# Performance work log

Hardware: AMD Instinct MI355X
Metric: run time of the kernel (lower is better)

## Reference

```python
import jax, jax.numpy as jnp
import numpy as np

EPS = 1e-8

def setup_inputs() -> dict:
    key = jax.random.key(0)
    k1, k2, k3, k4 = jax.random.split(key, 4)
    N, D = 65536, 384
    x_candidates = jax.random.normal(k1, (N, D), dtype=jnp.float32)
    y = jax.random.normal(k2, (D,), dtype=jnp.float32)
    z = jax.random.normal(k3, (D,), dtype=jnp.float32)
    a = jax.random.normal(k4, (D, D, D), dtype=jnp.float32)
    return {"x_candidates": x_candidates, "y": y, "z": z, "a": a}

def reference(x_candidates, y, z, a):
    # feature_fn is identity: fy = y, fz = z, fx = each candidate row.
    fy, fz = y, z
    # context[i] = sum_{j,k} a[i,j,k] * fy[j] * fz[k]  (the triple loop, fused)
    # computed as two matvecs to avoid materializing a*fy*fz outer products:
    # tmp[i,j] = sum_k a[i,j,k] * fz[k]; context[i] = sum_j tmp[i,j] * fy[j]
    context = jnp.einsum("ij,j->i", jnp.einsum("ijk,k->ij", a, fz), fy)  # [D]
    # denominator = sum_{j,k} a[0,j,k]*fy[j]*fz[k] == context[0]
    denominator = context[0]
    # score(x) = sum_i fx[i] * context[i] / (denominator + eps)
    scores = (x_candidates @ context) / (denominator + EPS)  # [N]
    return scores
```

## Files before the change

kernel.cpp:

```cpp
#include <hip/hip_runtime.h>

#define EPS 1e-8f

constexpr int D = 384;
constexpr int Q_PER_I = (D * D) / 4;
constexpr int P = 4;
constexpr int Q_PER_PART = Q_PER_I / P;
constexpr int THREADS_A = 256;
constexpr int ITERS_A = Q_PER_PART / THREADS_A;
constexpr int J_PER_PART = Q_PER_PART / (D / 4);

__global__ __launch_bounds__(THREADS_A) void ctx_partial_kernel(
    const float* __restrict__ a,
    const float* __restrict__ y,
    const float* __restrict__ z,
    float* __restrict__ partials) {
  const int b = blockIdx.x;
  const int i = b / P;
  const int part = b - i * P;
  const float4* a4 = reinterpret_cast<const float4*>(a) +
                     (size_t)i * Q_PER_I + (size_t)part * Q_PER_PART;
  const float4* z4 = reinterpret_cast<const float4*>(z);
  const int jbase = part * J_PER_PART;
  const int tid = threadIdx.x;

  float acc = 0.0f;
#pragma unroll 4
  for (int it = 0; it < ITERS_A; ++it) {
    int q = it * THREADS_A + tid;
    int jl = q / 96;
    int k4 = q - jl * 96;
    float4 av = a4[q];
    float4 zv = z4[k4];
    float yj = y[jbase + jl];
    acc += yj * (av.x * zv.x + av.y * zv.y + av.z * zv.z + av.w * zv.w);
  }

  for (int off = 32; off > 0; off >>= 1)
    acc += __shfl_down(acc, off);

  __shared__ float sm[THREADS_A / 64];
  const int lane = tid & 63;
  const int w = tid >> 6;
  if (lane == 0) sm[w] = acc;
  __syncthreads();
  if (tid == 0) {
    float s = 0.0f;
#pragma unroll
    for (int k = 0; k < THREADS_A / 64; ++k) s += sm[k];
    partials[i * P + part] = s;
  }
}

__global__ __launch_bounds__(D) void ctx_finalize_kernel(
    const float* __restrict__ partials,
    float* __restrict__ ctx_scaled) {
  __shared__ float denom_s;
  const int i = threadIdx.x;
  float s = 0.0f;
#pragma unroll
  for (int p = 0; p < P; ++p) s += partials[i * P + p];
  if (i == 0) denom_s = s;
  __syncthreads();
  const float scale = 1.0f / (denom_s + EPS);
  ctx_scaled[i] = s * scale;
}

__global__ __launch_bounds__(256) void score_kernel(
    const float* __restrict__ x,
    const float* __restrict__ ctx,
    float* __restrict__ out) {
  const int tid = threadIdx.x;
  const int lane = tid & 63;
  const int w = tid >> 6;
  const int row = blockIdx.x * 4 + w;
  const float4* xr = reinterpret_cast<const float4*>(x) + (size_t)row * (D / 4);
  const float4* c4 = reinterpret_cast<const float4*>(ctx);

  float4 xv = xr[lane];
  float4 cv = c4[lane];
  float s = xv.x * cv.x + xv.y * cv.y + xv.z * cv.z + xv.w * cv.w;
  if (lane < 32) {
    float4 xv2 = xr[64 + lane];
    float4 cv2 = c4[64 + lane];
    s += xv2.x * cv2.x + xv2.y * cv2.y + xv2.z * cv2.z + xv2.w * cv2.w;
  }
  for (int off = 32; off > 0; off >>= 1)
    s += __shfl_down(s, off);
  if (lane == 0) out[row] = s;
}

extern "C" void kernel_launch(void* const* d_in, const int* in_sizes, int n_in,
                              void* d_out, int out_size, void* d_ws, size_t ws_size,
                              hipStream_t stream) {
  const float* x = (const float*)d_in[0];
  const float* y = (const float*)d_in[1];
  const float* z = (const float*)d_in[2];
  const float* a = (const float*)d_in[3];
  float* out = (float*)d_out;

  const int N = in_sizes[0] / D;

  float* partials = (float*)d_ws;
  float* ctx = partials + D * P;

  ctx_partial_kernel<<<D * P, THREADS_A, 0, stream>>>(a, y, z, partials);
  ctx_finalize_kernel<<<1, D, 0, stream>>>(partials, ctx);
  score_kernel<<<N / 4, 256, 0, stream>>>(x, ctx, out);
}
```

Before: 63.11 us.

## Fuse context reduction and scoring into one cooperative persistent kernel

Replaces the three launches (partial context, finalize, score) with a single cooperative kernel of 1024 blocks. Each block first computes three of the context partial sums, then waits at a grid-wide barrier. After that, every block rebuilds the full context in shared memory and runs a grid-stride loop over candidate rows, applying the scale at the output. This removes two kernel launches and their gaps, and keeps the context vector in LDS. The cost is a grid.sync, redundant finalize work in every block, and a fixed grid size that must fit co-resident on the device.

```diff
diff --git a/kernel.cpp b/kernel.cpp
--- a/kernel.cpp
+++ b/kernel.cpp
@@ -1,93 +1,102 @@
 #include <hip/hip_runtime.h>
+#include <hip/hip_cooperative_groups.h>
+
+namespace cg = cooperative_groups;
 
 #define EPS 1e-8f
 
 constexpr int D = 384;
+constexpr int P = 8;
+constexpr int UNITS = D * P;
 constexpr int Q_PER_I = (D * D) / 4;
-constexpr int P = 4;
-constexpr int Q_PER_PART = Q_PER_I / P;
-constexpr int THREADS_A = 256;
-constexpr int ITERS_A = Q_PER_PART / THREADS_A;
-constexpr int J_PER_PART = Q_PER_PART / (D / 4);
+constexpr int Q_PER_UNIT = Q_PER_I / P;
+constexpr int THREADS = 256;
+constexpr int ITERS = Q_PER_UNIT / THREADS;
+constexpr int J_PER_UNIT = (D / P);
+constexpr int GRID = 1024;
+constexpr int UNITS_PER_BLOCK = UNITS / GRID;
 
-__global__ __launch_bounds__(THREADS_A) void ctx_partial_kernel(
-    const float* __restrict__ a,
+__global__ __launch_bounds__(THREADS, 4) void fused_kernel(
+    const float* __restrict__ x,
     const float* __restrict__ y,
     const float* __restrict__ z,
-    float* __restrict__ partials) {
+    const float* __restrict__ a,
+    float* __restrict__ partials,
+    float* __restrict__ out,
+    int N) {
+  cg::grid_group grid = cg::this_grid();
+
   const int b = blockIdx.x;
-  const int i = b / P;
-  const int part = b - i * P;
-  const float4* a4 = reinterpret_cast<const float4*>(a) +
-                     (size_t)i * Q_PER_I + (size_t)part * Q_PER_PART;
-  const float4* z4 = reinterpret_cast<const float4*>(z);
-  const int jbase = part * J_PER_PART;
-  const int tid = threadIdx.x;
-
-  float acc = 0.0f;
-#pragma unroll 4
-  for (int it = 0; it < ITERS_A; ++it) {
-    int q = it * THREADS_A + tid;
-    int jl = q / 96;
-    int k4 = q - jl * 96;
-    float4 av = a4[q];
-    float4 zv = z4[k4];
-    float yj = y[jbase + jl];
-    acc += yj * (av.x * zv.x + av.y * zv.y + av.z * zv.z + av.w * zv.w);
-  }
-
-  for (int off = 32; off > 0; off >>= 1)
-    acc += __shfl_down(acc, off);
-
-  __shared__ float sm[THREADS_A / 64];
-  const int lane = tid & 63;
-  const int w = tid >> 6;
-  if (lane == 0) sm[w] = acc;
-  __syncthreads();
-  if (tid == 0) {
-    float s = 0.0f;
-#pragma unroll
-    for (int k = 0; k < THREADS_A / 64; ++k) s += sm[k];
-    partials[i * P + part] = s;
-  }
-}
-
-__global__ __launch_bounds__(D) void ctx_finalize_kernel(
-    const float* __restrict__ partials,
-    float* __restrict__ ctx_scaled) {
-  __shared__ float denom_s;
-  const int i = threadIdx.x;
-  float s = 0.0f;
-#pragma unroll
-  for (int p = 0; p < P; ++p) s += partials[i * P + p];
-  if (i == 0) denom_s = s;
-  __syncthreads();
-  const float scale = 1.0f / (denom_s + EPS);
-  ctx_scaled[i] = s * scale;
-}
-
-__global__ __launch_bounds__(256) void score_kernel(
-    const float* __restrict__ x,
-    const float* __restrict__ ctx,
-    float* __restrict__ out) {
   const int tid = threadIdx.x;
   const int lane = tid & 63;
   const int w = tid >> 6;
-  const int row = blockIdx.x * 4 + w;
-  const float4* xr = reinterpret_cast<const float4*>(x) + (size_t)row * (D / 4);
-  const float4* c4 = reinterpret_cast<const float4*>(ctx);
 
-  float4 xv = xr[lane];
-  float4 cv = c4[lane];
-  float s = xv.x * cv.x + xv.y * cv.y + xv.z * cv.z + xv.w * cv.w;
-  if (lane < 32) {
-    float4 xv2 = xr[64 + lane];
-    float4 cv2 = c4[64 + lane];
-    s += xv2.x * cv2.x + xv2.y * cv2.y + xv2.z * cv2.z + xv2.w * cv2.w;
+  __shared__ float sm[THREADS / 64];
+  __shared__ float ctx_s[D];
+
+  const float4* z4 = reinterpret_cast<const float4*>(z);
+
+#pragma unroll
+  for (int ui = 0; ui < UNITS_PER_BLOCK; ++ui) {
+    const int unit = b + ui * GRID;
+    const int i = unit >> 3;
+    const int part = unit & 7;
+    const float4* a4 = reinterpret_cast<const float4*>(a) +
+                       (size_t)i * Q_PER_I + (size_t)part * Q_PER_UNIT;
+    const int jbase = part * J_PER_UNIT;
+
+    float acc = 0.0f;
+#pragma unroll 6
+    for (int it = 0; it < ITERS; ++it) {
+      int q = it * THREADS + tid;
+      int jl = q / 96;
+      int k4 = q - jl * 96;
+      float4 av = a4[q];
+      float4 zv = z4[k4];
+      float yj = y[jbase + jl];
+      acc += yj * (av.x * zv.x + av.y * zv.y + av.z * zv.z + av.w * zv.w);
+    }
+    for (int off = 32; off > 0; off >>= 1)
+      acc += __shfl_down(acc, off);
+    if (lane == 0) sm[w] = acc;
+    __syncthreads();
+    if (tid == 0) {
+      float s = 0.0f;
+#pragma unroll
+      for (int k = 0; k < THREADS / 64; ++k) s += sm[k];
+      partials[unit] = s;
+    }
+    __syncthreads();
   }
-  for (int off = 32; off > 0; off >>= 1)
-    s += __shfl_down(s, off);
-  if (lane == 0) out[row] = s;
+
+  grid.sync();
+
+  for (int t = tid; t < D; t += THREADS) {
+    float s = 0.0f;
+#pragma unroll
+    for (int p = 0; p < P; ++p) s += partials[t * P + p];
+    ctx_s[t] = s;
+  }
+  __syncthreads();
+  const float scale = 1.0f / (ctx_s[0] + EPS);
+  const float4* c4 = reinterpret_cast<const float4*>(ctx_s);
+  const float4 cv = c4[lane];
+  float4 cv2 = make_float4(0.f, 0.f, 0.f, 0.f);
+  if (lane < 32) cv2 = c4[64 + lane];
+
+  const int wavesTotal = GRID * (THREADS / 64);
+  for (int row = b * (THREADS / 64) + w; row < N; row += wavesTotal) {
+    const float4* xr = reinterpret_cast<const float4*>(x) + (size_t)row * (D / 4);
+    float4 xv = xr[lane];
+    float s = xv.x * cv.x + xv.y * cv.y + xv.z * cv.z + xv.w * cv.w;
+    if (lane < 32) {
+      float4 xv2 = xr[64 + lane];
+      s += xv2.x * cv2.x + xv2.y * cv2.y + xv2.z * cv2.z + xv2.w * cv2.w;
+    }
+    for (int off = 32; off > 0; off >>= 1)
+      s += __shfl_down(s, off);
+    if (lane == 0) out[row] = s * scale;
+  }
 }
 
 extern "C" void kernel_launch(void* const* d_in, const int* in_sizes, int n_in,
@@ -99,12 +108,11 @@
   const float* a = (const float*)d_in[3];
   float* out = (float*)d_out;
 
-  const int N = in_sizes[0] / D;
+  int N = in_sizes[0] / D;
+  float* partials = (float*)d_ws;
 
-  float* partials = (float*)d_ws;
-  float* ctx = partials + D * P;
-
-  ctx_partial_kernel<<<D * P, THREADS_A, 0, stream>>>(a, y, z, partials);
-  ctx_finalize_kernel<<<1, D, 0, stream>>>(partials, ctx);
-  score_kernel<<<N / 4, 256, 0, stream>>>(x, ctx, out);
+  void* args[] = {(void*)&x, (void*)&y, (void*)&z, (void*)&a,
+                  (void*)&partials, (void*)&out, (void*)&N};
+  hipLaunchCooperativeKernel((void*)fused_kernel, dim3(GRID), dim3(THREADS),
+                             args, 0, stream);
 }
```

Result: slower. 159.6 us (+152.9%).
